# Kernel tuning notes

Measured on AMD Instinct MI355X. Metric: run time of the kernel, lower is better.

## Reference

```python
import jax, jax.numpy as jnp
import numpy as np

B, M, IN, OUT = 4096, 8, 512, 512


def setup_inputs() -> dict:
    key = jax.random.key(0)
    k1, k2 = jax.random.split(key)
    x = jax.random.normal(k1, (B, M, IN), dtype=jnp.float32)
    # xavier_uniform over (n_mode, in, out): fan_in=IN, fan_out=OUT
    limit = float(np.sqrt(6.0 / (IN + OUT)))
    weight = jax.random.uniform(k2, (M, IN, OUT), dtype=jnp.float32,
                                minval=-limit, maxval=limit)
    bias = jnp.zeros((M, OUT), dtype=jnp.float32)
    return {"input": x, "weight": weight, "bias": bias}


def reference(input, weight, bias):
    # torch: (weight * input.unsqueeze(-1)).sum(-2) + bias
    # == per-mode linear: out[b,m,o] = sum_i input[b,m,i] * weight[m,i,o] + bias[m,o]
    out = jnp.einsum('bmi,mio->bmo', input, weight)
    return out + bias
```

## Files before the change

kernel.cpp:

```cpp
#include <hip/hip_runtime.h>
#include <hip/hip_bf16.h>


#define B_   4096
#define M_   8
#define IN_  512
#define OUT_ 512
#define BM   128
#define BN   128
#define BK   32
#define NKT  (IN_ / BK)
#define WS_NEED (M_ * 4 * 16 * 8192)

typedef __attribute__((ext_vector_type(8))) short  short8;
typedef __attribute__((ext_vector_type(4))) float  f32x4;
typedef __attribute__((ext_vector_type(4))) int    i32x4;

#define GLB(p) ((const __attribute__((address_space(1))) void*)(p))
#define LDS(p) ((__attribute__((address_space(3))) void*)(p))

static __device__ inline unsigned f2bf2(float lo, float hi) {
  union { float f; unsigned u; } a, b;
  a.f = lo; b.f = hi;
  unsigned ua = a.u + 0x7FFFu + ((a.u >> 16) & 1u);
  unsigned ub = b.u + 0x7FFFu + ((b.u >> 16) & 1u);
  return (ua >> 16) | (ub & 0xFFFF0000u);
}

union pk8 { i32x4 i; short8 s; };

extern "C" __global__ __launch_bounds__(256, 2)
void prep_w(const float* __restrict__ W, unsigned char* __restrict__ ws) {
  const int c  = blockIdx.x;
  const int kb = c & 15;
  const int nbm = c >> 4;
  const int nb = nbm & 3;
  const int m  = nbm >> 2;

  __shared__ float tile[32][132];

  const int t  = threadIdx.x;
  {
    const int k  = t >> 3;
    const int n4 = (t & 7) * 16;
    const float* src = W + (size_t)m * (IN_ * OUT_) + (size_t)(kb * 32 + k) * OUT_ + nb * 128 + n4;
#pragma unroll
    for (int i = 0; i < 4; ++i) {
      f32x4 v = *(const f32x4*)(src + i * 4);
      tile[k][n4 + i * 4 + 0] = v[0];
      tile[k][n4 + i * 4 + 1] = v[1];
      tile[k][n4 + i * 4 + 2] = v[2];
      tile[k][n4 + i * 4 + 3] = v[3];
    }
  }
  __syncthreads();

  unsigned char* out = ws + (size_t)c * 8192;
#pragma unroll
  for (int s = t; s < 512; s += 256) {
    const int col = s >> 2;
    const int k8  = s & 3;
    float f[8];
#pragma unroll
    for (int j = 0; j < 8; ++j) f[j] = tile[k8 * 8 + j][col];
    i32x4 p;
    p[0] = f2bf2(f[0], f[1]); p[1] = f2bf2(f[2], f[3]);
    p[2] = f2bf2(f[4], f[5]); p[3] = f2bf2(f[6], f[7]);
    const int phys = (col * 64 + k8 * 16) ^ ((col & 7) << 4);
    *(i32x4*)(out + phys) = p;
  }
}

extern "C" __global__ __launch_bounds__(256, 3)
void mmlin_main(const float* __restrict__ X, const unsigned char* __restrict__ Wp,
                const float* __restrict__ Bias, float* __restrict__ O) {
  __shared__ unsigned char lds[49152];

  const int t = threadIdx.x, l = t & 63, w = t >> 6;
  const int b0 = blockIdx.x * BM;
  const int nb = blockIdx.y;
  const int n0 = nb * BN;
  const int m  = blockIdx.z;

  const char* Xb = (const char*)X;
  const char* a_src[4];
  int a_dst[4];
#pragma unroll
  for (int i = 0; i < 4; ++i) {
    const int j = w * 4 + i;
    a_src[i] = Xb + (size_t)(b0 + j * 8 + (l >> 3)) * (M_ * IN_ * 4)
             + m * (IN_ * 4)
             + (((l & 7) ^ (l >> 3)) << 4);
    a_dst[i] = j * 1024 + l * 16;
  }
  const unsigned char* b_src = Wp + (size_t)((m * 4 + nb) * 16) * 8192 + (w * 2) * 1024 + l * 16;
  const int b_dst = 32768 + (w * 2) * 1024 + l * 16;

  const int wr = (w >> 1) * 64, wc = (w & 1) * 64;
  const int fr = l & 15, g = l >> 4;
  int aoff0[4], aoff1[4], boff[4];
#pragma unroll
  for (int mi = 0; mi < 4; ++mi) {
    const int row = wr + mi * 16 + fr;
    aoff0[mi] = row * 128 + (((2 * g)     ^ (row & 7)) << 4);
    aoff1[mi] = row * 128 + (((2 * g + 1) ^ (row & 7)) << 4);
  }
#pragma unroll
  for (int ni = 0; ni < 4; ++ni) {
    const int col = wc + ni * 16 + fr;
    boff[ni] = 32768 + ((col * 64 + g * 16) ^ ((col & 7) << 4));
  }

  f32x4 acc[4][4] = {};

#pragma unroll
  for (int i = 0; i < 4; ++i)
    __builtin_amdgcn_global_load_lds(GLB(a_src[i]), LDS(lds + a_dst[i]), 16, 0, 0);
#pragma unroll
  for (int i = 0; i < 2; ++i)
    __builtin_amdgcn_global_load_lds(GLB(b_src + i * 1024), LDS(lds + b_dst + i * 1024), 16, 0, 0);

  for (int kt = 0; kt < NKT; ++kt) {
    __syncthreads();
    const int cur = kt & 1;
    const int nxt = cur ^ 1;

    if (kt + 1 < NKT) {
#pragma unroll
      for (int i = 0; i < 4; ++i)
        __builtin_amdgcn_global_load_lds(GLB(a_src[i] + (kt + 1) * (BK * 4)),
                                         LDS(lds + nxt * 16384 + a_dst[i]), 16, 0, 0);
#pragma unroll
      for (int i = 0; i < 2; ++i)
        __builtin_amdgcn_global_load_lds(GLB(b_src + (size_t)(kt + 1) * 8192 + i * 1024),
                                         LDS(lds + nxt * 8192 + b_dst + i * 1024), 16, 0, 0);
    }

    const unsigned char* A  = lds + cur * 16384;
    const unsigned char* Bb = lds + cur * 8192;

    short8 af[4], bf[4];
#pragma unroll
    for (int mi = 0; mi < 4; ++mi) {
      f32x4 q0 = *(const f32x4*)(A + aoff0[mi]);
      f32x4 q1 = *(const f32x4*)(A + aoff1[mi]);
      pk8 p;
      p.i[0] = f2bf2(q0[0], q0[1]); p.i[1] = f2bf2(q0[2], q0[3]);
      p.i[2] = f2bf2(q1[0], q1[1]); p.i[3] = f2bf2(q1[2], q1[3]);
      af[mi] = p.s;
    }
#pragma unroll
    for (int ni = 0; ni < 4; ++ni)
      bf[ni] = *(const short8*)(Bb + boff[ni]);

#pragma unroll
    for (int mi = 0; mi < 4; ++mi)
#pragma unroll
      for (int ni = 0; ni < 4; ++ni)
        acc[mi][ni] = __builtin_amdgcn_mfma_f32_16x16x32_bf16(
            af[mi], bf[ni], acc[mi][ni], 0, 0, 0);
  }

#pragma unroll
  for (int ni = 0; ni < 4; ++ni) {
    const int col = n0 + wc + ni * 16 + fr;
    const float bs = Bias[m * OUT_ + col];
#pragma unroll
    for (int mi = 0; mi < 4; ++mi) {
#pragma unroll
      for (int r = 0; r < 4; ++r) {
        const int row = b0 + wr + mi * 16 + g * 4 + r;
        O[(size_t)row * (M_ * OUT_) + m * OUT_ + col] = acc[mi][ni][r] + bs;
      }
    }
  }
}

extern "C" __global__ __launch_bounds__(256, 2)
void mmlin_fallback(const float* __restrict__ X, const float* __restrict__ W,
                    const float* __restrict__ Bias, float* __restrict__ O) {
  __shared__ unsigned char lds[16384];
  const int t = threadIdx.x;
  const int lane = t & 63;
  const int w = t >> 6;
  const int b0 = blockIdx.x * BM;
  const int n0 = blockIdx.y * BN;
  const int m  = blockIdx.z;

  const int ar  = t >> 1;
  const int ac0 = (t & 1) * 16;
  const float* aptr = X + (size_t)(b0 + ar) * (M_ * IN_) + m * IN_ + ac0;
  const int swzA  = (ar & 7) << 4;
  const int a_st0 = (ar * 64 + ac0 * 2)      ^ swzA;
  const int a_st1 = (ar * 64 + ac0 * 2 + 16) ^ swzA;

  const int bc  = t & 127;
  const int bk0 = (t >> 7) * 16;
  const float* bptr = W + (size_t)m * IN_ * OUT_ + (size_t)bk0 * OUT_ + n0 + bc;
  const int swzB  = (bc & 7) << 4;
  const int b_st0 = (8192 + bc * 64 + bk0 * 2)      ^ swzB;
  const int b_st1 = (8192 + bc * 64 + bk0 * 2 + 16) ^ swzB;

  const int wr = (w >> 1) * 64, wc = (w & 1) * 64;
  const int fr = lane & 15;
  const int fkB = (lane >> 4) * 16;

  int a_ld[4], b_ld[4];
#pragma unroll
  for (int mi = 0; mi < 4; ++mi) {
    int row = wr + mi * 16 + fr;
    a_ld[mi] = (row * 64 + fkB) ^ ((row & 7) << 4);
  }
#pragma unroll
  for (int ni = 0; ni < 4; ++ni) {
    int col = wc + ni * 16 + fr;
    b_ld[ni] = (8192 + col * 64 + fkB) ^ ((col & 7) << 4);
  }

  f32x4 acc[4][4] = {};
  f32x4 a_raw[4];
  float b_raw[16];
  {
    const f32x4* ap = (const f32x4*)aptr;
#pragma unroll
    for (int i = 0; i < 4; ++i) a_raw[i] = ap[i];
#pragma unroll
    for (int j = 0; j < 16; ++j) b_raw[j] = bptr[(size_t)j * OUT_];
  }
  i32x4 apk0, apk1, bpk0, bpk1;
  apk0[0] = f2bf2(a_raw[0][0], a_raw[0][1]); apk0[1] = f2bf2(a_raw[0][2], a_raw[0][3]);
  apk0[2] = f2bf2(a_raw[1][0], a_raw[1][1]); apk0[3] = f2bf2(a_raw[1][2], a_raw[1][3]);
  apk1[0] = f2bf2(a_raw[2][0], a_raw[2][1]); apk1[1] = f2bf2(a_raw[2][2], a_raw[2][3]);
  apk1[2] = f2bf2(a_raw[3][0], a_raw[3][1]); apk1[3] = f2bf2(a_raw[3][2], a_raw[3][3]);
  bpk0[0] = f2bf2(b_raw[0],  b_raw[1]);  bpk0[1] = f2bf2(b_raw[2],  b_raw[3]);
  bpk0[2] = f2bf2(b_raw[4],  b_raw[5]);  bpk0[3] = f2bf2(b_raw[6],  b_raw[7]);
  bpk1[0] = f2bf2(b_raw[8],  b_raw[9]);  bpk1[1] = f2bf2(b_raw[10], b_raw[11]);
  bpk1[2] = f2bf2(b_raw[12], b_raw[13]); bpk1[3] = f2bf2(b_raw[14], b_raw[15]);

  for (int kk = 0; kk < IN_; kk += BK) {
    __syncthreads();
    *(i32x4*)(lds + a_st0) = apk0;
    *(i32x4*)(lds + a_st1) = apk1;
    *(i32x4*)(lds + b_st0) = bpk0;
    *(i32x4*)(lds + b_st1) = bpk1;
    __syncthreads();

    const int kn = kk + BK;
    if (kn < IN_) {
      const f32x4* ap = (const f32x4*)(aptr + kn);
#pragma unroll
      for (int i = 0; i < 4; ++i) a_raw[i] = ap[i];
#pragma unroll
      for (int j = 0; j < 16; ++j) b_raw[j] = bptr[(size_t)(kn + j) * OUT_];
    }

    short8 af[4], bf4[4];
#pragma unroll
    for (int mi = 0; mi < 4; ++mi) af[mi]  = *(const short8*)(lds + a_ld[mi]);
#pragma unroll
    for (int ni = 0; ni < 4; ++ni) bf4[ni] = *(const short8*)(lds + b_ld[ni]);

#pragma unroll
    for (int mi = 0; mi < 4; ++mi)
#pragma unroll
      for (int ni = 0; ni < 4; ++ni)
        acc[mi][ni] = __builtin_amdgcn_mfma_f32_16x16x32_bf16(
            af[mi], bf4[ni], acc[mi][ni], 0, 0, 0);

    if (kn < IN_) {
      apk0[0] = f2bf2(a_raw[0][0], a_raw[0][1]); apk0[1] = f2bf2(a_raw[0][2], a_raw[0][3]);
      apk0[2] = f2bf2(a_raw[1][0], a_raw[1][1]); apk0[3] = f2bf2(a_raw[1][2], a_raw[1][3]);
      apk1[0] = f2bf2(a_raw[2][0], a_raw[2][1]); apk1[1] = f2bf2(a_raw[2][2], a_raw[2][3]);
      apk1[2] = f2bf2(a_raw[3][0], a_raw[3][1]); apk1[3] = f2bf2(a_raw[3][2], a_raw[3][3]);
      bpk0[0] = f2bf2(b_raw[0],  b_raw[1]);  bpk0[1] = f2bf2(b_raw[2],  b_raw[3]);
      bpk0[2] = f2bf2(b_raw[4],  b_raw[5]);  bpk0[3] = f2bf2(b_raw[6],  b_raw[7]);
      bpk1[0] = f2bf2(b_raw[8],  b_raw[9]);  bpk1[1] = f2bf2(b_raw[10], b_raw[11]);
      bpk1[2] = f2bf2(b_raw[12], b_raw[13]); bpk1[3] = f2bf2(b_raw[14], b_raw[15]);
    }
  }

#pragma unroll
  for (int ni = 0; ni < 4; ++ni) {
    const int col = n0 + wc + ni * 16 + fr;
    const float bs = Bias[m * OUT_ + col];
#pragma unroll
    for (int mi = 0; mi < 4; ++mi) {
#pragma unroll
      for (int r = 0; r < 4; ++r) {
        const int row = b0 + wr + mi * 16 + (lane >> 4) * 4 + r;
        O[(size_t)row * (M_ * OUT_) + m * OUT_ + col] = acc[mi][ni][r] + bs;
      }
    }
  }
}

extern "C" void kernel_launch(void* const* d_in, const int* in_sizes, int n_in,
                              void* d_out, int out_size, void* d_ws, size_t ws_size,
                              hipStream_t stream) {
  const float* X    = (const float*)d_in[0];
  const float* W    = (const float*)d_in[1];
  const float* Bias = (const float*)d_in[2];
  float* O = (float*)d_out;

  dim3 grid(B_ / BM, OUT_ / BN, M_);
  if (ws_size >= (size_t)WS_NEED) {
    prep_w<<<dim3(512), dim3(256), 0, stream>>>(W, (unsigned char*)d_ws);
    mmlin_main<<<grid, dim3(256), 0, stream>>>(X, (const unsigned char*)d_ws, Bias, O);
  } else {
    mmlin_fallback<<<grid, dim3(256), 0, stream>>>(X, W, Bias, O);
  }
}
```

Before: 153.2 us.

## Load activation fragments directly to registers with deeper prefetch, keep only B in LDS

The main GEMM kernel no longer stages fp32 activations through LDS. Each wave now loads its 32 rows of X straight into registers two k-steps ahead and converts them to bf16 fragments. Only the pre-packed bf16 weights stay double-buffered in LDS, and the warp tile changes from 64x64 to 32x128, so each wave reads all B columns. The loop is fully unrolled with manual vmcnt/lgkmcnt waits and raw barriers, and bf16 conversion uses the HIP intrinsic. This cuts LDS footprint and traffic, which may raise occupancy, but the direct fragment loads are less coalesced and register pressure goes up.

```diff
diff --git a/kernel.cpp b/kernel.cpp
--- a/kernel.cpp
+++ b/kernel.cpp
@@ -6,28 +6,33 @@
 #define M_   8
 #define IN_  512
 #define OUT_ 512
-#define BM   128
-#define BN   128
 #define BK   32
-#define NKT  (IN_ / BK)
+#define NKT  16
 #define WS_NEED (M_ * 4 * 16 * 8192)
 
 typedef __attribute__((ext_vector_type(8))) short  short8;
 typedef __attribute__((ext_vector_type(4))) float  f32x4;
 typedef __attribute__((ext_vector_type(4))) int    i32x4;
 
-#define GLB(p) ((const __attribute__((address_space(1))) void*)(p))
-#define LDS(p) ((__attribute__((address_space(3))) void*)(p))
+#define GLB(p)  ((const __attribute__((address_space(1))) void*)(p))
+#define LDSP(p) ((__attribute__((address_space(3))) void*)(p))
+#define FENCE() asm volatile("" ::: "memory")
 
 static __device__ inline unsigned f2bf2(float lo, float hi) {
-  union { float f; unsigned u; } a, b;
-  a.f = lo; b.f = hi;
-  unsigned ua = a.u + 0x7FFFu + ((a.u >> 16) & 1u);
-  unsigned ub = b.u + 0x7FFFu + ((b.u >> 16) & 1u);
-  return (ua >> 16) | (ub & 0xFFFF0000u);
+  float2 f2; f2.x = lo; f2.y = hi;
+  __hip_bfloat162 h = __float22bfloat162_rn(f2);
+  union { __hip_bfloat162 h; unsigned u; } c; c.h = h;
+  return c.u;
 }
 
 union pk8 { i32x4 i; short8 s; };
+
+static __device__ inline short8 cvt8(f32x4 a, f32x4 b) {
+  pk8 p;
+  p.i[0] = f2bf2(a[0], a[1]); p.i[1] = f2bf2(a[2], a[3]);
+  p.i[2] = f2bf2(b[0], b[1]); p.i[3] = f2bf2(b[2], b[3]);
+  return p.s;
+}
 
 extern "C" __global__ __launch_bounds__(256, 2)
 void prep_w(const float* __restrict__ W, unsigned char* __restrict__ ws) {
@@ -39,7 +44,7 @@
 
   __shared__ float tile[32][132];
 
-  const int t  = threadIdx.x;
+  const int t = threadIdx.x;
   {
     const int k  = t >> 3;
     const int n4 = (t & 7) * 16;
@@ -74,102 +79,115 @@
 extern "C" __global__ __launch_bounds__(256, 3)
 void mmlin_main(const float* __restrict__ X, const unsigned char* __restrict__ Wp,
                 const float* __restrict__ Bias, float* __restrict__ O) {
-  __shared__ unsigned char lds[49152];
+  __shared__ unsigned char ldsB[16384];
 
   const int t = threadIdx.x, l = t & 63, w = t >> 6;
-  const int b0 = blockIdx.x * BM;
+  const int b0 = blockIdx.x * 128;
   const int nb = blockIdx.y;
-  const int n0 = nb * BN;
+  const int n0 = nb * 128;
   const int m  = blockIdx.z;
-
-  const char* Xb = (const char*)X;
-  const char* a_src[4];
-  int a_dst[4];
-#pragma unroll
-  for (int i = 0; i < 4; ++i) {
-    const int j = w * 4 + i;
-    a_src[i] = Xb + (size_t)(b0 + j * 8 + (l >> 3)) * (M_ * IN_ * 4)
-             + m * (IN_ * 4)
-             + (((l & 7) ^ (l >> 3)) << 4);
-    a_dst[i] = j * 1024 + l * 16;
-  }
-  const unsigned char* b_src = Wp + (size_t)((m * 4 + nb) * 16) * 8192 + (w * 2) * 1024 + l * 16;
-  const int b_dst = 32768 + (w * 2) * 1024 + l * 16;
-
-  const int wr = (w >> 1) * 64, wc = (w & 1) * 64;
   const int fr = l & 15, g = l >> 4;
-  int aoff0[4], aoff1[4], boff[4];
-#pragma unroll
-  for (int mi = 0; mi < 4; ++mi) {
-    const int row = wr + mi * 16 + fr;
-    aoff0[mi] = row * 128 + (((2 * g)     ^ (row & 7)) << 4);
-    aoff1[mi] = row * 128 + (((2 * g + 1) ^ (row & 7)) << 4);
-  }
-#pragma unroll
-  for (int ni = 0; ni < 4; ++ni) {
-    const int col = wc + ni * 16 + fr;
-    boff[ni] = 32768 + ((col * 64 + g * 16) ^ ((col & 7) << 4));
-  }
-
-  f32x4 acc[4][4] = {};
-
-#pragma unroll
-  for (int i = 0; i < 4; ++i)
-    __builtin_amdgcn_global_load_lds(GLB(a_src[i]), LDS(lds + a_dst[i]), 16, 0, 0);
-#pragma unroll
-  for (int i = 0; i < 2; ++i)
-    __builtin_amdgcn_global_load_lds(GLB(b_src + i * 1024), LDS(lds + b_dst + i * 1024), 16, 0, 0);
-
-  for (int kt = 0; kt < NKT; ++kt) {
-    __syncthreads();
-    const int cur = kt & 1;
-    const int nxt = cur ^ 1;
-
-    if (kt + 1 < NKT) {
-#pragma unroll
-      for (int i = 0; i < 4; ++i)
-        __builtin_amdgcn_global_load_lds(GLB(a_src[i] + (kt + 1) * (BK * 4)),
-                                         LDS(lds + nxt * 16384 + a_dst[i]), 16, 0, 0);
-#pragma unroll
-      for (int i = 0; i < 2; ++i)
-        __builtin_amdgcn_global_load_lds(GLB(b_src + (size_t)(kt + 1) * 8192 + i * 1024),
-                                         LDS(lds + nxt * 8192 + b_dst + i * 1024), 16, 0, 0);
-    }
-
-    const unsigned char* A  = lds + cur * 16384;
-    const unsigned char* Bb = lds + cur * 8192;
-
-    short8 af[4], bf[4];
-#pragma unroll
-    for (int mi = 0; mi < 4; ++mi) {
-      f32x4 q0 = *(const f32x4*)(A + aoff0[mi]);
-      f32x4 q1 = *(const f32x4*)(A + aoff1[mi]);
-      pk8 p;
-      p.i[0] = f2bf2(q0[0], q0[1]); p.i[1] = f2bf2(q0[2], q0[3]);
-      p.i[2] = f2bf2(q1[0], q1[1]); p.i[3] = f2bf2(q1[2], q1[3]);
-      af[mi] = p.s;
-    }
-#pragma unroll
-    for (int ni = 0; ni < 4; ++ni)
-      bf[ni] = *(const short8*)(Bb + boff[ni]);
-
-#pragma unroll
-    for (int mi = 0; mi < 4; ++mi)
-#pragma unroll
-      for (int ni = 0; ni < 4; ++ni)
-        acc[mi][ni] = __builtin_amdgcn_mfma_f32_16x16x32_bf16(
-            af[mi], bf[ni], acc[mi][ni], 0, 0, 0);
-  }
-
-#pragma unroll
-  for (int ni = 0; ni < 4; ++ni) {
-    const int col = n0 + wc + ni * 16 + fr;
+
+  const float* aptr[2];
+#pragma unroll
+  for (int mi = 0; mi < 2; ++mi)
+    aptr[mi] = X + (size_t)(b0 + w * 32 + mi * 16 + fr) * (M_ * IN_) + m * IN_ + g * 8;
+
+  const unsigned char* b_src = Wp + (size_t)((m * 4 + nb) * 16) * 8192 + w * 2048 + l * 16;
+  const int b_dst = w * 2048 + l * 16;
+
+  int boff[8];
+#pragma unroll
+  for (int ni = 0; ni < 8; ++ni) {
+    const int col = ni * 16 + fr;
+    boff[ni] = (col * 64 + g * 16) ^ ((col & 7) << 4);
+  }
+
+  f32x4 acc[2][8] = {};
+  f32x4 slot[2][4];
+  short8 af[2][2];
+
+  FENCE();
+  __builtin_amdgcn_global_load_lds(GLB(b_src),        LDSP(ldsB + b_dst),        16, 0, 0);
+  __builtin_amdgcn_global_load_lds(GLB(b_src + 1024), LDSP(ldsB + b_dst + 1024), 16, 0, 0);
+  FENCE();
+#pragma unroll
+  for (int mi = 0; mi < 2; ++mi) {
+    slot[0][mi * 2 + 0] = *(const f32x4*)(aptr[mi] + 0);
+    slot[0][mi * 2 + 1] = *(const f32x4*)(aptr[mi] + 4);
+  }
+  FENCE();
+#pragma unroll
+  for (int mi = 0; mi < 2; ++mi) {
+    slot[1][mi * 2 + 0] = *(const f32x4*)(aptr[mi] + BK + 0);
+    slot[1][mi * 2 + 1] = *(const f32x4*)(aptr[mi] + BK + 4);
+  }
+  FENCE();
+  af[0][0] = cvt8(slot[0][0], slot[0][1]);
+  af[0][1] = cvt8(slot[0][2], slot[0][3]);
+  asm volatile("s_waitcnt vmcnt(4)" ::: "memory");
+  asm volatile("s_waitcnt lgkmcnt(0)" ::: "memory");
+  __builtin_amdgcn_s_barrier();
+  __builtin_amdgcn_sched_barrier(0);
+
+#pragma unroll
+  for (int k = 0; k < NKT; ++k) {
+    if (k + 1 < NKT) {
+      FENCE();
+      const unsigned char* bs = b_src + (size_t)(k + 1) * 8192;
+      const int bd = ((k + 1) & 1) * 8192 + b_dst;
+      __builtin_amdgcn_global_load_lds(GLB(bs),        LDSP(ldsB + bd),        16, 0, 0);
+      __builtin_amdgcn_global_load_lds(GLB(bs + 1024), LDSP(ldsB + bd + 1024), 16, 0, 0);
+    }
+    if (k + 2 < NKT) {
+      FENCE();
+#pragma unroll
+      for (int mi = 0; mi < 2; ++mi) {
+        slot[k & 1][mi * 2 + 0] = *(const f32x4*)(aptr[mi] + (k + 2) * BK + 0);
+        slot[k & 1][mi * 2 + 1] = *(const f32x4*)(aptr[mi] + (k + 2) * BK + 4);
+      }
+    }
+    FENCE();
+
+    const unsigned char* Bbuf = ldsB + (k & 1) * 8192;
+    short8 bf0[4], bf1[4];
+#pragma unroll
+    for (int j = 0; j < 4; ++j) bf0[j] = *(const short8*)(Bbuf + boff[j]);
+#pragma unroll
+    for (int mi = 0; mi < 2; ++mi)
+#pragma unroll
+      for (int j = 0; j < 4; ++j)
+        acc[mi][j] = __builtin_amdgcn_mfma_f32_16x16x32_bf16(
+            af[k & 1][mi], bf0[j], acc[mi][j], 0, 0, 0);
+#pragma unroll
+    for (int j = 0; j < 4; ++j) bf1[j] = *(const short8*)(Bbuf + boff[4 + j]);
+#pragma unroll
+    for (int mi = 0; mi < 2; ++mi)
+#pragma unroll
+      for (int j = 0; j < 4; ++j)
+        acc[mi][4 + j] = __builtin_amdgcn_mfma_f32_16x16x32_bf16(
+            af[k & 1][mi], bf1[j], acc[mi][4 + j], 0, 0, 0);
+
+    if (k + 1 < NKT) {
+      af[(k + 1) & 1][0] = cvt8(slot[(k + 1) & 1][0], slot[(k + 1) & 1][1]);
+      af[(k + 1) & 1][1] = cvt8(slot[(k + 1) & 1][2], slot[(k + 1) & 1][3]);
+      if (k <= NKT - 3) { asm volatile("s_waitcnt vmcnt(4)" ::: "memory"); }
+      else              { asm volatile("s_waitcnt vmcnt(0)" ::: "memory"); }
+      asm volatile("s_waitcnt lgkmcnt(0)" ::: "memory");
+      __builtin_amdgcn_s_barrier();
+      __builtin_amdgcn_sched_barrier(0);
+    }
+  }
+
+#pragma unroll
+  for (int ni = 0; ni < 8; ++ni) {
+    const int col = n0 + ni * 16 + fr;
     const float bs = Bias[m * OUT_ + col];
 #pragma unroll
-    for (int mi = 0; mi < 4; ++mi) {
+    for (int mi = 0; mi < 2; ++mi) {
 #pragma unroll
       for (int r = 0; r < 4; ++r) {
-        const int row = b0 + wr + mi * 16 + g * 4 + r;
+        const int row = b0 + w * 32 + mi * 16 + g * 4 + r;
         O[(size_t)row * (M_ * OUT_) + m * OUT_ + col] = acc[mi][ni][r] + bs;
       }
     }
@@ -183,8 +201,8 @@
   const int t = threadIdx.x;
   const int lane = t & 63;
   const int w = t >> 6;
-  const int b0 = blockIdx.x * BM;
-  const int n0 = blockIdx.y * BN;
+  const int b0 = blockIdx.x * 128;
+  const int n0 = blockIdx.y * 128;
   const int m  = blockIdx.z;
 
   const int ar  = t >> 1;
@@ -302,7 +320,7 @@
   const float* Bias = (const float*)d_in[2];
   float* O = (float*)d_out;
 
-  dim3 grid(B_ / BM, OUT_ / BN, M_);
+  dim3 grid(B_ / 128, OUT_ / 128, M_);
   if (ws_size >= (size_t)WS_NEED) {
     prep_w<<<dim3(512), dim3(256), 0, stream>>>(W, (unsigned char*)d_ws);
     mmlin_main<<<grid, dim3(256), 0, stream>>>(X, (const unsigned char*)d_ws, Bias, O);
```

Result: slower. 162.9 us (+6.3%).

## Halve batch tile, raise occupancy, reorder grid, and move prefetch after LDS reads

Applied to the files above, without the earlier changes.

Shrinks the main kernel's batch tile from 128 to 64 rows, which cuts LDS use to 32 KB and lets the launch bound request 4 blocks per CU instead of 3. The grid now puts the output-column block on x, so the 4 blocks that share the same X rows run next to each other and can reuse them from L2. The next-stage global-to-LDS prefetch is now issued after the current fragments are read rather than before. The bf16 pack now uses the HIP float2-to-bfloat162 intrinsic. The trade-off is that each wave does half as many MFMAs per tile, so LDS-read and sync overhead per FLOP goes up.

```diff
diff --git a/kernel.cpp b/kernel.cpp
--- a/kernel.cpp
+++ b/kernel.cpp
@@ -6,28 +6,32 @@
 #define M_   8
 #define IN_  512
 #define OUT_ 512
-#define BM   128
-#define BN   128
 #define BK   32
-#define NKT  (IN_ / BK)
+#define NKT  16
 #define WS_NEED (M_ * 4 * 16 * 8192)
 
 typedef __attribute__((ext_vector_type(8))) short  short8;
 typedef __attribute__((ext_vector_type(4))) float  f32x4;
 typedef __attribute__((ext_vector_type(4))) int    i32x4;
 
-#define GLB(p) ((const __attribute__((address_space(1))) void*)(p))
-#define LDS(p) ((__attribute__((address_space(3))) void*)(p))
+#define GLB(p)  ((const __attribute__((address_space(1))) void*)(p))
+#define LDSP(p) ((__attribute__((address_space(3))) void*)(p))
 
 static __device__ inline unsigned f2bf2(float lo, float hi) {
-  union { float f; unsigned u; } a, b;
-  a.f = lo; b.f = hi;
-  unsigned ua = a.u + 0x7FFFu + ((a.u >> 16) & 1u);
-  unsigned ub = b.u + 0x7FFFu + ((b.u >> 16) & 1u);
-  return (ua >> 16) | (ub & 0xFFFF0000u);
+  float2 f2; f2.x = lo; f2.y = hi;
+  __hip_bfloat162 h = __float22bfloat162_rn(f2);
+  union { __hip_bfloat162 h; unsigned u; } c; c.h = h;
+  return c.u;
 }
 
 union pk8 { i32x4 i; short8 s; };
+
+static __device__ inline short8 cvt8(f32x4 a, f32x4 b) {
+  pk8 p;
+  p.i[0] = f2bf2(a[0], a[1]); p.i[1] = f2bf2(a[2], a[3]);
+  p.i[2] = f2bf2(b[0], b[1]); p.i[3] = f2bf2(b[2], b[3]);
+  return p.s;
+}
 
 extern "C" __global__ __launch_bounds__(256, 2)
 void prep_w(const float* __restrict__ W, unsigned char* __restrict__ ws) {
@@ -39,7 +43,7 @@
 
   __shared__ float tile[32][132];
 
-  const int t  = threadIdx.x;
+  const int t = threadIdx.x;
   {
     const int k  = t >> 3;
     const int n4 = (t & 7) * 16;
@@ -71,36 +75,38 @@
   }
 }
 
-extern "C" __global__ __launch_bounds__(256, 3)
+extern "C" __global__ __launch_bounds__(256, 4)
 void mmlin_main(const float* __restrict__ X, const unsigned char* __restrict__ Wp,
                 const float* __restrict__ Bias, float* __restrict__ O) {
-  __shared__ unsigned char lds[49152];
+  __shared__ unsigned char lds[32768];
 
   const int t = threadIdx.x, l = t & 63, w = t >> 6;
-  const int b0 = blockIdx.x * BM;
-  const int nb = blockIdx.y;
-  const int n0 = nb * BN;
+  const int nb = blockIdx.x;
+  const int b0 = blockIdx.y * 64;
   const int m  = blockIdx.z;
+  const int n0 = nb * 128;
+  const int fr = l & 15, g = l >> 4;
 
   const char* Xb = (const char*)X;
-  const char* a_src[4];
-  int a_dst[4];
-#pragma unroll
-  for (int i = 0; i < 4; ++i) {
-    const int j = w * 4 + i;
-    a_src[i] = Xb + (size_t)(b0 + j * 8 + (l >> 3)) * (M_ * IN_ * 4)
-             + m * (IN_ * 4)
+  const char* a_src[2];
+  int a_dst[2];
+#pragma unroll
+  for (int i = 0; i < 2; ++i) {
+    const int issue = w * 2 + i;
+    const int r     = issue * 8 + (l >> 3);
+    a_src[i] = Xb + (size_t)(b0 + r) * (M_ * IN_ * 4) + m * (IN_ * 4)
              + (((l & 7) ^ (l >> 3)) << 4);
-    a_dst[i] = j * 1024 + l * 16;
-  }
-  const unsigned char* b_src = Wp + (size_t)((m * 4 + nb) * 16) * 8192 + (w * 2) * 1024 + l * 16;
-  const int b_dst = 32768 + (w * 2) * 1024 + l * 16;
-
-  const int wr = (w >> 1) * 64, wc = (w & 1) * 64;
-  const int fr = l & 15, g = l >> 4;
-  int aoff0[4], aoff1[4], boff[4];
-#pragma unroll
-  for (int mi = 0; mi < 4; ++mi) {
+    a_dst[i] = issue * 1024 + l * 16;
+  }
+
+  const unsigned char* b_src = Wp + (size_t)((m * 4 + nb) * 16) * 8192 + w * 2048 + l * 16;
+  const int b_dst = 16384 + w * 2048 + l * 16;
+
+  const int wr = (w >> 1) * 32;
+  const int wc = (w & 1) * 64;
+  int aoff0[2], aoff1[2], boff[4];
+#pragma unroll
+  for (int mi = 0; mi < 2; ++mi) {
     const int row = wr + mi * 16 + fr;
     aoff0[mi] = row * 128 + (((2 * g)     ^ (row & 7)) << 4);
     aoff1[mi] = row * 128 + (((2 * g + 1) ^ (row & 7)) << 4);
@@ -108,53 +114,49 @@
 #pragma unroll
   for (int ni = 0; ni < 4; ++ni) {
     const int col = wc + ni * 16 + fr;
-    boff[ni] = 32768 + ((col * 64 + g * 16) ^ ((col & 7) << 4));
-  }
-
-  f32x4 acc[4][4] = {};
-
-#pragma unroll
-  for (int i = 0; i < 4; ++i)
-    __builtin_amdgcn_global_load_lds(GLB(a_src[i]), LDS(lds + a_dst[i]), 16, 0, 0);
+    boff[ni] = 16384 + ((col * 64 + g * 16) ^ ((col & 7) << 4));
+  }
+
+  f32x4 acc[2][4] = {};
+
 #pragma unroll
   for (int i = 0; i < 2; ++i)
-    __builtin_amdgcn_global_load_lds(GLB(b_src + i * 1024), LDS(lds + b_dst + i * 1024), 16, 0, 0);
+    __builtin_amdgcn_global_load_lds(GLB(a_src[i]), LDSP(lds + a_dst[i]), 16, 0, 0);
+  __builtin_amdgcn_global_load_lds(GLB(b_src),        LDSP(lds + b_dst),        16, 0, 0);
+  __builtin_amdgcn_global_load_lds(GLB(b_src + 1024), LDSP(lds + b_dst + 1024), 16, 0, 0);
 
   for (int kt = 0; kt < NKT; ++kt) {
     __syncthreads();
     const int cur = kt & 1;
-    const int nxt = cur ^ 1;
-
-    if (kt + 1 < NKT) {
-#pragma unroll
-      for (int i = 0; i < 4; ++i)
-        __builtin_amdgcn_global_load_lds(GLB(a_src[i] + (kt + 1) * (BK * 4)),
-                                         LDS(lds + nxt * 16384 + a_dst[i]), 16, 0, 0);
-#pragma unroll
-      for (int i = 0; i < 2; ++i)
-        __builtin_amdgcn_global_load_lds(GLB(b_src + (size_t)(kt + 1) * 8192 + i * 1024),
-                                         LDS(lds + nxt * 8192 + b_dst + i * 1024), 16, 0, 0);
-    }
-
-    const unsigned char* A  = lds + cur * 16384;
+
+    const unsigned char* A  = lds + cur * 8192;
     const unsigned char* Bb = lds + cur * 8192;
 
-    short8 af[4], bf[4];
-#pragma unroll
-    for (int mi = 0; mi < 4; ++mi) {
+    short8 af[2], bf[4];
+#pragma unroll
+    for (int mi = 0; mi < 2; ++mi) {
       f32x4 q0 = *(const f32x4*)(A + aoff0[mi]);
       f32x4 q1 = *(const f32x4*)(A + aoff1[mi]);
-      pk8 p;
-      p.i[0] = f2bf2(q0[0], q0[1]); p.i[1] = f2bf2(q0[2], q0[3]);
-      p.i[2] = f2bf2(q1[0], q1[1]); p.i[3] = f2bf2(q1[2], q1[3]);
-      af[mi] = p.s;
+      af[mi] = cvt8(q0, q1);
     }
 #pragma unroll
     for (int ni = 0; ni < 4; ++ni)
       bf[ni] = *(const short8*)(Bb + boff[ni]);
 
-#pragma unroll
-    for (int mi = 0; mi < 4; ++mi)
+    if (kt + 1 < NKT) {
+      const int nx = (kt + 1) & 1;
+#pragma unroll
+      for (int i = 0; i < 2; ++i)
+        __builtin_amdgcn_global_load_lds(GLB(a_src[i] + (kt + 1) * (BK * 4)),
+                                         LDSP(lds + nx * 8192 + a_dst[i]), 16, 0, 0);
+      __builtin_amdgcn_global_load_lds(GLB(b_src + (size_t)(kt + 1) * 8192),
+                                       LDSP(lds + nx * 8192 + b_dst), 16, 0, 0);
+      __builtin_amdgcn_global_load_lds(GLB(b_src + (size_t)(kt + 1) * 8192 + 1024),
+                                       LDSP(lds + nx * 8192 + b_dst + 1024), 16, 0, 0);
+    }
+
+#pragma unroll
+    for (int mi = 0; mi < 2; ++mi)
 #pragma unroll
       for (int ni = 0; ni < 4; ++ni)
         acc[mi][ni] = __builtin_amdgcn_mfma_f32_16x16x32_bf16(
@@ -166,7 +168,7 @@
     const int col = n0 + wc + ni * 16 + fr;
     const float bs = Bias[m * OUT_ + col];
 #pragma unroll
-    for (int mi = 0; mi < 4; ++mi) {
+    for (int mi = 0; mi < 2; ++mi) {
 #pragma unroll
       for (int r = 0; r < 4; ++r) {
         const int row = b0 + wr + mi * 16 + g * 4 + r;
@@ -183,8 +185,8 @@
   const int t = threadIdx.x;
   const int lane = t & 63;
   const int w = t >> 6;
-  const int b0 = blockIdx.x * BM;
-  const int n0 = blockIdx.y * BN;
+  const int b0 = blockIdx.x * 128;
+  const int n0 = blockIdx.y * 128;
   const int m  = blockIdx.z;
 
   const int ar  = t >> 1;
@@ -302,11 +304,12 @@
   const float* Bias = (const float*)d_in[2];
   float* O = (float*)d_out;
 
-  dim3 grid(B_ / BM, OUT_ / BN, M_);
   if (ws_size >= (size_t)WS_NEED) {
     prep_w<<<dim3(512), dim3(256), 0, stream>>>(W, (unsigned char*)d_ws);
+    dim3 grid(OUT_ / 128, B_ / 64, M_);
     mmlin_main<<<grid, dim3(256), 0, stream>>>(X, (const unsigned char*)d_ws, Bias, O);
   } else {
+    dim3 grid(B_ / 128, OUT_ / 128, M_);
     mmlin_fallback<<<grid, dim3(256), 0, stream>>>(X, W, Bias, O);
   }
 }
```

Measured after the change: 163.1 us. 1.06x slower.
